# Kernel tuning notes

Hardware: AMD Instinct MI355X
Metric: run time of the kernel (lower is better)

The kernel has to match this reference:

```python
import jax, jax.numpy as jnp
import numpy as np

TOPK = 3
IOU_THRESHOLD = 0.5


def setup_inputs() -> dict:
    key = jax.random.key(0)
    k0, k1, k2, k3 = jax.random.split(key, 4)
    S, N, TGT_PER_VID = 256, 128, 4
    M = S * TGT_PER_VID          # 1024 target moments total
    P = N * N                    # 16384 valid proposals (mask2d all ones)
    start_offset = jax.random.normal(k0, (S, P), dtype=jnp.float32) * 0.1
    end_offset = jax.random.normal(k1, (S, P), dtype=jnp.float32) * 0.1
    # target moments: (start, end) in [0,1], start <= end
    tgt_moments = jnp.sort(jax.random.uniform(k2, (M, 2), dtype=jnp.float32), axis=1)
    num_targets = jnp.full((S,), TGT_PER_VID, dtype=jnp.int32)  # sums to M
    iou2ds = jax.random.uniform(k3, (M, N, N), dtype=jnp.float32)
    mask2d = jnp.ones((N, N), dtype=bool)
    return {
        "start_offset": start_offset,
        "end_offset": end_offset,
        "tgt_moments": tgt_moments,
        "num_targets": num_targets,
        "iou2ds": iou2ds,
        "mask2d": mask2d,
    }


def reference(start_offset, end_offset, tgt_moments, num_targets, iou2ds, mask2d):
    M, N, _ = iou2ds.shape
    S, P = start_offset.shape
    # map each of the M targets back to its source video (repeat_interleave)
    scatter_m2s = jnp.repeat(jnp.arange(S), num_targets, total_repeat_length=M)
    so = start_offset[scatter_m2s]  # [M, P]
    eo = end_offset[scatter_m2s]    # [M, P]
    # row-major nonzero positions of mask2d (== torch masked_select ordering)
    rows, cols = jnp.nonzero(mask2d, size=P)
    iou1ds = iou2ds[:, rows, cols]  # [M, P]
    # top-k scatter mask + IoU-threshold mask
    _, topk_idx = jax.lax.top_k(iou1ds, TOPK)  # [M, TOPK]
    target_mask = jnp.zeros((M, P), dtype=start_offset.dtype)
    target_mask = target_mask.at[jnp.arange(M)[:, None], topk_idx].set(1.0)
    target_mask = jnp.where(iou1ds > IOU_THRESHOLD, 1.0, target_mask)
    # scores2ds_to_moments: proposal (row, col) -> moment (row/N, (col+1)/N)
    starts = rows.astype(start_offset.dtype) / N                 # [P]
    ends = (cols.astype(start_offset.dtype) + 1.0) / N           # [P]
    start_offset_target = tgt_moments[:, 0:1] - starts[None, :]  # [M, P]
    end_offset_target = tgt_moments[:, 1:2] - ends[None, :]      # [M, P]
    loss = jnp.abs(so - start_offset_target) + jnp.abs(eo - end_offset_target)
    return (loss * target_mask).sum() / target_mask.sum()
```

## Files before the change

### kernel.cpp

```cpp
#include <hip/hip_runtime.h>
#include <math.h>

#define TOPK_N 3
#define IOU_THR 0.5f
#define NCNT 8
#define THREADS 512
#define NW (THREADS / 64)
#define SENT 0x7fffffff

__device__ __forceinline__ bool better(float va, int ia, float vb, int ib) {
    return (va > vb) || (va == vb && ia < ib);
}

__device__ __forceinline__ void merge3(float& a0, float& a1, float& a2,
                                       int& x0, int& x1, int& x2,
                                       float b0, float b1, float b2,
                                       int y0, int y1, int y2) {
    bool t0 = better(a0, x0, b0, y0);
    float ov0 = t0 ? a0 : b0;  int oi0 = t0 ? x0 : y0;
    float ahv = t0 ? a1 : a0;  int ahi = t0 ? x1 : x0;
    float a2v = t0 ? a2 : a1;  int a2i = t0 ? x2 : x1;
    float bhv = t0 ? b0 : b1;  int bhi = t0 ? y0 : y1;
    float b2v = t0 ? b1 : b2;  int b2i = t0 ? y1 : y2;
    bool t1 = better(ahv, ahi, bhv, bhi);
    float ov1 = t1 ? ahv : bhv; int oi1 = t1 ? ahi : bhi;
    float cav = t1 ? a2v : ahv; int cai = t1 ? a2i : ahi;
    float cbv = t1 ? bhv : b2v; int cbi = t1 ? bhi : b2i;
    bool t2 = better(cav, cai, cbv, cbi);
    a0 = ov0; a1 = ov1; a2 = t2 ? cav : cbv;
    x0 = oi0; x1 = oi1; x2 = t2 ? cai : cbi;
}

__global__ void prep_kernel(const int* __restrict__ num_targets,
                            const int* __restrict__ mask2d,
                            int* __restrict__ scatter,
                            int* __restrict__ counts,
                            int S, int M, int P) {
    const int bid = blockIdx.x;
    const int tid = threadIdx.x;

    if (bid < NCNT) {
        const int P4 = P >> 2;
        const int4* __restrict__ m4 = (const int4*)mask2d;
        int c = 0;
        for (int q = bid * 256 + tid; q < P4; q += NCNT * 256) {
            const int4 v = m4[q];
            c += (v.x != 0) + (v.y != 0) + (v.z != 0) + (v.w != 0);
        }
        if (bid == 0) {
            for (int j = (P4 << 2) + tid; j < P; j += 256)
                c += (mask2d[j] != 0);
        }
        __shared__ int red[256];
        red[tid] = c;
        __syncthreads();
        for (int st = 128; st > 0; st >>= 1) {
            if (tid < st) red[tid] += red[tid + st];
            __syncthreads();
        }
        if (tid == 0) counts[bid] = red[0];
    } else {
        __shared__ int cum[1025];
        __shared__ int scn[256];
        const int chunk = (S + 255) / 256;
        const int sbase = tid * chunk;
        int local[4];
        int csum = 0;
        for (int k = 0; k < chunk && k < 4; ++k) {
            int s = sbase + k;
            int v = (s < S) ? num_targets[s] : 0;
            csum += v;
            local[k] = csum;
        }
        scn[tid] = csum;
        __syncthreads();
        for (int d = 1; d < 256; d <<= 1) {
            int v = scn[tid];
            int add = (tid >= d) ? scn[tid - d] : 0;
            __syncthreads();
            scn[tid] = v + add;
            __syncthreads();
        }
        {
            int excl = scn[tid] - csum;
            for (int k = 0; k < chunk && k < 4; ++k) {
                int s = sbase + k;
                if (s < S) cum[s + 1] = excl + local[k];
            }
            if (tid == 0) cum[0] = 0;
        }
        __syncthreads();
        const int total = cum[S];
        for (int m = tid; m < M; m += 256) {
            int mm = m;
            if (mm >= total) mm = (total > 0) ? (total - 1) : 0;
            int lo = 0, hi = S - 1;
            while (lo < hi) {
                int mid = (lo + hi) >> 1;
                if (cum[mid + 1] <= mm) lo = mid + 1; else hi = mid;
            }
            scatter[m] = lo;
        }
    }
}

__global__ void build_kernel(const int* __restrict__ counts,
                             const int* __restrict__ mask2d,
                             int* __restrict__ rcidx,
                             float* __restrict__ starts,
                             float* __restrict__ ends,
                             int* __restrict__ flag,
                             int N, int P) {
    const int tid = threadIdx.x;
    __shared__ int scan[256];

    scan[tid] = (tid < NCNT) ? counts[tid] : 0;
    __syncthreads();
    for (int st = 128; st > 0; st >>= 1) {
        if (tid < st) scan[tid] += scan[tid + st];
        __syncthreads();
    }
    const int K_all = scan[0];
    const int f = (K_all == P && (P & 3) == 0 && (N & (N - 1)) == 0 && N >= 4) ? 1 : 0;
    if (tid == 0) flag[0] = f;
    if (f) return;
    __syncthreads();

    const int per = (P + 255) / 256;
    const int base = tid * per;
    int cnt = 0;
    for (int k = 0; k < per; ++k) {
        int j = base + k;
        if (j < P && mask2d[j] != 0) cnt++;
    }
    scan[tid] = cnt;
    __syncthreads();
    for (int d = 1; d < 256; d <<= 1) {
        int v = scan[tid];
        int add = (tid >= d) ? scan[tid - d] : 0;
        __syncthreads();
        scan[tid] = v + add;
        __syncthreads();
    }
    const int K = scan[255];
    int pos = scan[tid] - cnt;

    const float fN = (float)N;
    for (int k = 0; k < per; ++k) {
        int j = base + k;
        if (j < P && mask2d[j] != 0) {
            int r = j / N;
            int c = j - r * N;
            rcidx[pos]  = j;
            starts[pos] = (float)r / fN;
            ends[pos]   = (float)(c + 1) / fN;
            pos++;
        }
    }
    __syncthreads();
    for (int j = K + tid; j < P; j += 256) {
        rcidx[j]  = 0;
        starts[j] = 0.0f;
        ends[j]   = 1.0f / fN;
    }
}

__global__ __launch_bounds__(THREADS, 8)
void loss_kernel(const float* __restrict__ start_offset,
                 const float* __restrict__ end_offset,
                 const float* __restrict__ tgt_moments,
                 const int* __restrict__ scatter,
                 const float* __restrict__ iou2ds,
                 const int* __restrict__ rcidx,
                 const float* __restrict__ starts,
                 const float* __restrict__ ends,
                 double* __restrict__ psum,
                 int* __restrict__ pcnt,
                 const int* __restrict__ flag,
                 int P, int M, int N) {
    const int bid = blockIdx.x;
    const int m = ((M & 7) == 0) ? ((bid & 7) * (M >> 3) + (bid >> 3)) : bid;
    const int tid = threadIdx.x;
    const int s   = scatter[m];
    const int fp  = flag[0];

    const float* __restrict__ so_row  = start_offset + (size_t)s * P;
    const float* __restrict__ eo_row  = end_offset   + (size_t)s * P;
    const float* __restrict__ iou_row = iou2ds       + (size_t)m * P;
    const float tgt0 = tgt_moments[2 * m];
    const float tgt1 = tgt_moments[2 * m + 1];

    const int   lgN  = 31 - __clz(N);
    const float invN = 1.0f / (float)N;

    float lsum = 0.0f;
    int   lcnt = 0;

    float v0 = -INFINITY, v1 = -INFINITY, v2 = -INFINITY;
    int   i0 = SENT, i1 = SENT, i2 = SENT;

#define PROC(v, jj, so_, eo_, A_, B_)                                       \
    do {                                                                    \
        const bool b0 = (v) > v0;                                           \
        const bool b1 = (v) > v1;                                           \
        const bool b2 = (v) > v2;                                           \
        v2 = b1 ? v1 : (b2 ? (v) : v2);  i2 = b1 ? i1 : (b2 ? (jj) : i2);   \
        v1 = b0 ? v0 : (b1 ? (v) : v1);  i1 = b0 ? i0 : (b1 ? (jj) : i1);   \
        v0 = b0 ? (v) : v0;              i0 = b0 ? (jj) : i0;               \
        const bool sel = (v) > IOU_THR;                                     \
        const float l_ = fabsf((so_) - (A_)) + fabsf((eo_) - (B_));         \
        lsum += sel ? l_ : 0.0f;                                            \
        lcnt += sel ? 1 : 0;                                                \
    } while (0)

#define PROC4(vi, vs, ve, q)                                                \
    do {                                                                    \
        const int j_  = (q) << 2;                                           \
        const int r_  = j_ >> lgN;                                          \
        const int c_  = j_ & (N - 1);                                       \
        const float A_  = tgt0 - (float)r_ * invN;      \
        const float en0 = (float)(c_ + 1) * invN;     \
        PROC((vi).x, j_ + 0, (vs).x, (ve).x, A_, tgt1 - en0);               \
        PROC((vi).y, j_ + 1, (vs).y, (ve).y, A_, tgt1 - (en0 + invN));      \
        PROC((vi).z, j_ + 2, (vs).z, (ve).z, A_, tgt1 - (en0 + 2.0f*invN)); \
        PROC((vi).w, j_ + 3, (vs).w, (ve).w, A_, tgt1 - (en0 + 3.0f*invN)); \
    } while (0)

    if (fp && (P & (8 * THREADS - 1)) == 0) {
        const float4* __restrict__ iou4 = (const float4*)iou_row;
        const float4* __restrict__ so4  = (const float4*)so_row;
        const float4* __restrict__ eo4  = (const float4*)eo_row;
        const int ITERS = P >> (2 + 1 + 9);
        int qA = tid;
        for (int it = 0; it < ITERS; ++it) {
            const int qB = qA + THREADS;
            const float4 iA = iou4[qA]; const float4 iB = iou4[qB];
            const float4 sA = so4[qA];  const float4 sB = so4[qB];
            const float4 eA = eo4[qA];  const float4 eB = eo4[qB];
            PROC4(iA, sA, eA, qA);
            PROC4(iB, sB, eB, qB);
            qA += 2 * THREADS;
        }
    } else if (fp) {
        const float4* __restrict__ iou4 = (const float4*)iou_row;
        const float4* __restrict__ so4  = (const float4*)so_row;
        const float4* __restrict__ eo4  = (const float4*)eo_row;
        const int P4 = P >> 2;
        for (int q = tid; q < P4; q += THREADS) {
            const float4 vi = iou4[q];
            const float4 vs = so4[q];
            const float4 ve = eo4[q];
            PROC4(vi, vs, ve, q);
        }
    } else {
        for (int j = tid; j < P; j += THREADS) {
            const int   idx = rcidx[j];
            const float v   = iou_row[idx];
            const float A_  = tgt0 - starts[j];
            const float B_  = tgt1 - ends[j];
            PROC(v, j, so_row[j], eo_row[j], A_, B_);
        }
    }
#undef PROC4
#undef PROC

    for (int d = 1; d < 64; d <<= 1) {
        float bv0 = __shfl_xor(v0, d), bv1 = __shfl_xor(v1, d), bv2 = __shfl_xor(v2, d);
        int   by0 = __shfl_xor(i0, d), by1 = __shfl_xor(i1, d), by2 = __shfl_xor(i2, d);
        merge3(v0, v1, v2, i0, i1, i2, bv0, bv1, bv2, by0, by1, by2);
    }
    double dsum = (double)lsum;
    for (int d = 1; d < 64; d <<= 1) dsum += __shfl_xor(dsum, d);
    for (int d = 1; d < 64; d <<= 1) lcnt += __shfl_xor(lcnt, d);

    __shared__ float  wv[NW][3];
    __shared__ int    wi[NW][3];
    __shared__ double wsum[NW];
    __shared__ int    wcnt[NW];
    const int wid  = tid >> 6;
    const int lane = tid & 63;
    if (lane == 0) {
        wv[wid][0] = v0; wv[wid][1] = v1; wv[wid][2] = v2;
        wi[wid][0] = i0; wi[wid][1] = i1; wi[wid][2] = i2;
        wsum[wid] = dsum; wcnt[wid] = lcnt;
    }
    __syncthreads();

    if (tid == 0) {
        float a0 = wv[0][0], a1 = wv[0][1], a2 = wv[0][2];
        int   x0 = wi[0][0], x1 = wi[0][1], x2 = wi[0][2];
        double S = wsum[0];
        int    C = wcnt[0];
        for (int w = 1; w < NW; ++w) {
            merge3(a0, a1, a2, x0, x1, x2,
                   wv[w][0], wv[w][1], wv[w][2],
                   wi[w][0], wi[w][1], wi[w][2]);
            S += wsum[w];
            C += wcnt[w];
        }
#define ADDTOP(vk, jk)                                                      \
        do {                                                                \
            if ((jk) != SENT && !((vk) > IOU_THR)) {                        \
                float st_, en_;                                             \
                if (fp) {                                                   \
                    int r_ = (jk) >> lgN, c_ = (jk) & (N - 1);              \
                    st_ = (float)r_ * invN; en_ = (float)(c_ + 1) * invN;   \
                } else { st_ = starts[jk]; en_ = ends[jk]; }                \
                S += (double)(fabsf(so_row[jk] - (tgt0 - st_)) +            \
                              fabsf(eo_row[jk] - (tgt1 - en_)));            \
                C += 1;                                                     \
            }                                                               \
        } while (0)
        ADDTOP(a0, x0);
        ADDTOP(a1, x1);
        ADDTOP(a2, x2);
#undef ADDTOP
        psum[bid] = S;
        pcnt[bid] = C;
    }
}

__global__ void finalize_kernel(const double* __restrict__ psum,
                                const int* __restrict__ pcnt,
                                int M, float* __restrict__ out) {
    __shared__ double sd[256];
    __shared__ int    sc[256];
    const int tid = threadIdx.x;
    double a = 0.0;
    int    c = 0;
    for (int i = tid; i < M; i += 256) { a += psum[i]; c += pcnt[i]; }
    sd[tid] = a; sc[tid] = c;
    __syncthreads();
    for (int str = 128; str > 0; str >>= 1) {
        if (tid < str) { sd[tid] += sd[tid + str]; sc[tid] += sc[tid + str]; }
        __syncthreads();
    }
    if (tid == 0) out[0] = (float)(sd[0] / (double)sc[0]);
}

extern "C" void kernel_launch(void* const* d_in, const int* in_sizes, int n_in,
                              void* d_out, int out_size, void* d_ws, size_t ws_size,
                              hipStream_t stream) {
    const float* start_offset = (const float*)d_in[0];
    const float* end_offset   = (const float*)d_in[1];
    const float* tgt_moments  = (const float*)d_in[2];
    const int*   num_targets  = (const int*)d_in[3];
    const float* iou2ds       = (const float*)d_in[4];
    const int*   mask2d       = (const int*)d_in[5];

    const int S = in_sizes[3];
    const int M = in_sizes[2] / 2;
    const int P = in_sizes[0] / S;
    const int NN = in_sizes[5];
    int N = 1;
    while ((long long)N * N < (long long)NN) N++;

    char* ws = (char*)d_ws;
    size_t off = 0;
    int*    flag    = (int*)(ws + off);    off += 16;
    int*    counts  = (int*)(ws + off);    off += (NCNT * 4 + 15) & ~(size_t)15;
    int*    scatter = (int*)(ws + off);    off += ((size_t)M * 4 + 15) & ~(size_t)15;
    int*    rcidx   = (int*)(ws + off);    off += ((size_t)P * 4 + 15) & ~(size_t)15;
    float*  starts  = (float*)(ws + off);  off += ((size_t)P * 4 + 15) & ~(size_t)15;
    float*  ends    = (float*)(ws + off);  off += ((size_t)P * 4 + 15) & ~(size_t)15;
    double* psum    = (double*)(ws + off); off += ((size_t)M * 8 + 15) & ~(size_t)15;
    int*    pcnt    = (int*)(ws + off);    off += ((size_t)M * 4 + 15) & ~(size_t)15;

    prep_kernel<<<NCNT + 1, 256, 0, stream>>>(num_targets, mask2d, scatter, counts,
                                              S, M, P);
    build_kernel<<<1, 256, 0, stream>>>(counts, mask2d, rcidx, starts, ends, flag, N, P);
    loss_kernel<<<M, THREADS, 0, stream>>>(start_offset, end_offset, tgt_moments,
                                           scatter, iou2ds, rcidx, starts, ends,
                                           psum, pcnt, flag, P, M, N);
    finalize_kernel<<<1, 256, 0, stream>>>(psum, pcnt, M, (float*)d_out);
}
```

Baseline: 34.55 us.

## Double-buffer float4 loads in main loop, use med3 for top-3 insertion

```diff
diff --git a/kernel.cpp b/kernel.cpp
--- a/kernel.cpp
+++ b/kernel.cpp
@@ -165,7 +165,7 @@
     }
 }
 
-__global__ __launch_bounds__(THREADS, 8)
+__global__ __launch_bounds__(THREADS, 4)
 void loss_kernel(const float* __restrict__ start_offset,
                  const float* __restrict__ end_offset,
                  const float* __restrict__ tgt_moments,
@@ -204,9 +204,13 @@
         const bool b0 = (v) > v0;                                           \
         const bool b1 = (v) > v1;                                           \
         const bool b2 = (v) > v2;                                           \
-        v2 = b1 ? v1 : (b2 ? (v) : v2);  i2 = b1 ? i1 : (b2 ? (jj) : i2);   \
-        v1 = b0 ? v0 : (b1 ? (v) : v1);  i1 = b0 ? i0 : (b1 ? (jj) : i1);   \
-        v0 = b0 ? (v) : v0;              i0 = b0 ? (jj) : i0;               \
+        const float nv0 = fmaxf(v0, (v));                                   \
+        const float nv1 = __builtin_amdgcn_fmed3f((v), v0, v1);             \
+        const float nv2 = __builtin_amdgcn_fmed3f((v), v1, v2);             \
+        i2 = b1 ? i1 : (b2 ? (jj) : i2);                                    \
+        i1 = b0 ? i0 : (b1 ? (jj) : i1);                                    \
+        i0 = b0 ? (jj) : i0;                                                \
+        v0 = nv0; v1 = nv1; v2 = nv2;                                       \
         const bool sel = (v) > IOU_THR;                                     \
         const float l_ = fabsf((so_) - (A_)) + fabsf((eo_) - (B_));         \
         lsum += sel ? l_ : 0.0f;                                            \
@@ -226,21 +230,48 @@
         PROC((vi).w, j_ + 3, (vs).w, (ve).w, A_, tgt1 - (en0 + 3.0f*invN)); \
     } while (0)
 
-    if (fp && (P & (8 * THREADS - 1)) == 0) {
+    if (fp && (P % (16 * THREADS)) == 0) {
         const float4* __restrict__ iou4 = (const float4*)iou_row;
         const float4* __restrict__ so4  = (const float4*)so_row;
         const float4* __restrict__ eo4  = (const float4*)eo_row;
-        const int ITERS = P >> (2 + 1 + 9);
-        int qA = tid;
-        for (int it = 0; it < ITERS; ++it) {
-            const int qB = qA + THREADS;
-            const float4 iA = iou4[qA]; const float4 iB = iou4[qB];
-            const float4 sA = so4[qA];  const float4 sB = so4[qB];
-            const float4 eA = eo4[qA];  const float4 eB = eo4[qB];
-            PROC4(iA, sA, eA, qA);
-            PROC4(iB, sB, eB, qB);
-            qA += 2 * THREADS;
-        }
+        const int G = P / (16 * THREADS);
+        float4 iA0, iA1, iA2, iA3, sA0, sA1, sA2, sA3, eA0, eA1, eA2, eA3;
+        float4 iB0, iB1, iB2, iB3, sB0, sB1, sB2, sB3, eB0, eB1, eB2, eB3;
+
+#define LOADG(T, g)                                                         \
+    do {                                                                    \
+        const int qb_ = (g) * (4 * THREADS) + tid;                          \
+        i##T##0 = iou4[qb_];               i##T##1 = iou4[qb_ + THREADS];   \
+        i##T##2 = iou4[qb_ + 2*THREADS];   i##T##3 = iou4[qb_ + 3*THREADS]; \
+        s##T##0 = so4[qb_];                s##T##1 = so4[qb_ + THREADS];    \
+        s##T##2 = so4[qb_ + 2*THREADS];    s##T##3 = so4[qb_ + 3*THREADS];  \
+        e##T##0 = eo4[qb_];                e##T##1 = eo4[qb_ + THREADS];    \
+        e##T##2 = eo4[qb_ + 2*THREADS];    e##T##3 = eo4[qb_ + 3*THREADS];  \
+    } while (0)
+
+#define COMPG(T, g)                                                         \
+    do {                                                                    \
+        const int qb_ = (g) * (4 * THREADS) + tid;                          \
+        PROC4(i##T##0, s##T##0, e##T##0, qb_);                              \
+        PROC4(i##T##1, s##T##1, e##T##1, qb_ + THREADS);                    \
+        PROC4(i##T##2, s##T##2, e##T##2, qb_ + 2*THREADS);                  \
+        PROC4(i##T##3, s##T##3, e##T##3, qb_ + 3*THREADS);                  \
+    } while (0)
+
+        LOADG(A, 0);
+        int g = 0;
+        while (true) {
+            if (g + 1 < G) LOADG(B, g + 1);
+            COMPG(A, g);
+            ++g;
+            if (g >= G) break;
+            if (g + 1 < G) LOADG(A, g + 1);
+            COMPG(B, g);
+            ++g;
+            if (g >= G) break;
+        }
+#undef COMPG
+#undef LOADG
     } else if (fp) {
         const float4* __restrict__ iou4 = (const float4*)iou_row;
         const float4* __restrict__ so4  = (const float4*)so_row;
```

Measured after the change: 51.42 us. 1.49x slower.

## Stage loss-kernel loads through LDS with async double buffering per wave

Applied to the files above, without the earlier changes.

```diff
diff --git a/kernel.cpp b/kernel.cpp
--- a/kernel.cpp
+++ b/kernel.cpp
@@ -1,11 +1,8 @@
 #include <hip/hip_runtime.h>
 #include <math.h>
 
-#define TOPK_N 3
 #define IOU_THR 0.5f
 #define NCNT 8
-#define THREADS 512
-#define NW (THREADS / 64)
 #define SENT 0x7fffffff
 
 __device__ __forceinline__ bool better(float va, int ia, float vb, int ib) {
@@ -31,6 +28,13 @@
     x0 = oi0; x1 = oi1; x2 = t2 ? cai : cbi;
 }
 
+__device__ __forceinline__ void gload16(const void* g, void* l) {
+    __builtin_amdgcn_global_load_lds(
+        (const __attribute__((address_space(1))) unsigned int*)g,
+        (__attribute__((address_space(3))) unsigned int*)l,
+        16, 0, 0);
+}
+
 __global__ void prep_kernel(const int* __restrict__ num_targets,
                             const int* __restrict__ mask2d,
                             int* __restrict__ scatter,
@@ -165,7 +169,7 @@
     }
 }
 
-__global__ __launch_bounds__(THREADS, 8)
+__global__ __launch_bounds__(256)
 void loss_kernel(const float* __restrict__ start_offset,
                  const float* __restrict__ end_offset,
                  const float* __restrict__ tgt_moments,
@@ -181,8 +185,8 @@
     const int bid = blockIdx.x;
     const int m = ((M & 7) == 0) ? ((bid & 7) * (M >> 3) + (bid >> 3)) : bid;
     const int tid = threadIdx.x;
+    const int fp  = flag[0];
     const int s   = scatter[m];
-    const int fp  = flag[0];
 
     const float* __restrict__ so_row  = start_offset + (size_t)s * P;
     const float* __restrict__ eo_row  = end_offset   + (size_t)s * P;
@@ -193,67 +197,103 @@
     const int   lgN  = 31 - __clz(N);
     const float invN = 1.0f / (float)N;
 
+    float v0 = -INFINITY, v1 = -INFINITY, v2 = -INFINITY;
+    int   i0 = SENT, i1 = SENT, i2 = SENT;
     float lsum = 0.0f;
     int   lcnt = 0;
-
-    float v0 = -INFINITY, v1 = -INFINITY, v2 = -INFINITY;
-    int   i0 = SENT, i1 = SENT, i2 = SENT;
 
 #define PROC(v, jj, so_, eo_, A_, B_)                                       \
     do {                                                                    \
         const bool b0 = (v) > v0;                                           \
         const bool b1 = (v) > v1;                                           \
         const bool b2 = (v) > v2;                                           \
-        v2 = b1 ? v1 : (b2 ? (v) : v2);  i2 = b1 ? i1 : (b2 ? (jj) : i2);   \
-        v1 = b0 ? v0 : (b1 ? (v) : v1);  i1 = b0 ? i0 : (b1 ? (jj) : i1);   \
-        v0 = b0 ? (v) : v0;              i0 = b0 ? (jj) : i0;               \
+        const float nv0 = fmaxf(v0, (v));                                   \
+        const float nv1 = __builtin_amdgcn_fmed3f((v), v0, v1);             \
+        const float nv2 = __builtin_amdgcn_fmed3f((v), v1, v2);             \
+        i2 = b1 ? i1 : (b2 ? (jj) : i2);                                    \
+        i1 = b0 ? i0 : (b1 ? (jj) : i1);                                    \
+        i0 = b0 ? (jj) : i0;                                                \
+        v0 = nv0; v1 = nv1; v2 = nv2;                                       \
         const bool sel = (v) > IOU_THR;                                     \
         const float l_ = fabsf((so_) - (A_)) + fabsf((eo_) - (B_));         \
         lsum += sel ? l_ : 0.0f;                                            \
         lcnt += sel ? 1 : 0;                                                \
     } while (0)
 
-#define PROC4(vi, vs, ve, q)                                                \
+#define PROC4(vi, vs, ve, qf4)                                              \
     do {                                                                    \
-        const int j_  = (q) << 2;                                           \
-        const int r_  = j_ >> lgN;                                          \
-        const int c_  = j_ & (N - 1);                                       \
-        const float A_  = tgt0 - (float)r_ * invN;      \
-        const float en0 = (float)(c_ + 1) * invN;     \
+        const int j_ = (qf4) << 2;                                          \
+        const int r_ = j_ >> lgN;                                           \
+        const int c_ = j_ & (N - 1);                                        \
+        const float A_  = tgt0 - (float)r_ * invN;                          \
+        const float en0 = (float)(c_ + 1) * invN;                           \
         PROC((vi).x, j_ + 0, (vs).x, (ve).x, A_, tgt1 - en0);               \
         PROC((vi).y, j_ + 1, (vs).y, (ve).y, A_, tgt1 - (en0 + invN));      \
         PROC((vi).z, j_ + 2, (vs).z, (ve).z, A_, tgt1 - (en0 + 2.0f*invN)); \
         PROC((vi).w, j_ + 3, (vs).w, (ve).w, A_, tgt1 - (en0 + 3.0f*invN)); \
     } while (0)
 
-    if (fp && (P & (8 * THREADS - 1)) == 0) {
-        const float4* __restrict__ iou4 = (const float4*)iou_row;
-        const float4* __restrict__ so4  = (const float4*)so_row;
-        const float4* __restrict__ eo4  = (const float4*)eo_row;
-        const int ITERS = P >> (2 + 1 + 9);
-        int qA = tid;
-        for (int it = 0; it < ITERS; ++it) {
-            const int qB = qA + THREADS;
-            const float4 iA = iou4[qA]; const float4 iB = iou4[qB];
-            const float4 sA = so4[qA];  const float4 sB = so4[qB];
-            const float4 eA = eo4[qA];  const float4 eB = eo4[qB];
-            PROC4(iA, sA, eA, qA);
-            PROC4(iB, sB, eB, qB);
-            qA += 2 * THREADS;
-        }
+    __shared__ float4 stg[4][2][3][128];
+
+    const bool deep = fp && ((P & 2047) == 0);
+
+    if (deep) {
+        const int wid  = tid >> 6;
+        const int lane = tid & 63;
+        const float4* __restrict__ io4 = (const float4*)iou_row;
+        const float4* __restrict__ so4 = (const float4*)so_row;
+        const float4* __restrict__ eo4 = (const float4*)eo_row;
+        const int wq0   = wid * (P >> 4);
+        const int iters = (P >> 4) >> 7;
+
+#define STAGE(B, T)                                                         \
+    do {                                                                    \
+        const int qb = wq0 + (T) * 128;                                     \
+        gload16(io4 + qb + lane,      &stg[wid][B][0][0]);                  \
+        gload16(io4 + qb + 64 + lane, &stg[wid][B][0][64]);                 \
+        gload16(so4 + qb + lane,      &stg[wid][B][1][0]);                  \
+        gload16(so4 + qb + 64 + lane, &stg[wid][B][1][64]);                 \
+        gload16(eo4 + qb + lane,      &stg[wid][B][2][0]);                  \
+        gload16(eo4 + qb + 64 + lane, &stg[wid][B][2][64]);                 \
+    } while (0)
+
+        STAGE(0, 0);
+        for (int t = 0; t < iters; ++t) {
+            const int b = t & 1;
+            if (t + 1 < iters) {
+                asm volatile("s_waitcnt lgkmcnt(0)" ::: "memory");
+                __builtin_amdgcn_sched_barrier(0);
+                STAGE(b ^ 1, t + 1);
+                asm volatile("s_waitcnt vmcnt(6)" ::: "memory");
+            } else {
+                asm volatile("s_waitcnt vmcnt(0)" ::: "memory");
+            }
+            __builtin_amdgcn_sched_barrier(0);
+
+            const int q  = wq0 + t * 128 + lane;
+            const float4 vi0 = stg[wid][b][0][lane];
+            const float4 vi1 = stg[wid][b][0][64 + lane];
+            const float4 vs0 = stg[wid][b][1][lane];
+            const float4 vs1 = stg[wid][b][1][64 + lane];
+            const float4 ve0 = stg[wid][b][2][lane];
+            const float4 ve1 = stg[wid][b][2][64 + lane];
+            PROC4(vi0, vs0, ve0, q);
+            PROC4(vi1, vs1, ve1, q + 64);
+        }
+#undef STAGE
     } else if (fp) {
-        const float4* __restrict__ iou4 = (const float4*)iou_row;
-        const float4* __restrict__ so4  = (const float4*)so_row;
-        const float4* __restrict__ eo4  = (const float4*)eo_row;
+        const float4* __restrict__ io4 = (const float4*)iou_row;
+        const float4* __restrict__ so4 = (const float4*)so_row;
+        const float4* __restrict__ eo4 = (const float4*)eo_row;
         const int P4 = P >> 2;
-        for (int q = tid; q < P4; q += THREADS) {
-            const float4 vi = iou4[q];
+        for (int q = tid; q < P4; q += 256) {
+            const float4 vi = io4[q];
             const float4 vs = so4[q];
             const float4 ve = eo4[q];
             PROC4(vi, vs, ve, q);
         }
     } else {
-        for (int j = tid; j < P; j += THREADS) {
+        for (int j = tid; j < P; j += 256) {
             const int   idx = rcidx[j];
             const float v   = iou_row[idx];
             const float A_  = tgt0 - starts[j];
@@ -265,18 +305,18 @@
 #undef PROC
 
     for (int d = 1; d < 64; d <<= 1) {
-        float bv0 = __shfl_xor(v0, d), bv1 = __shfl_xor(v1, d), bv2 = __shfl_xor(v2, d);
-        int   by0 = __shfl_xor(i0, d), by1 = __shfl_xor(i1, d), by2 = __shfl_xor(i2, d);
-        merge3(v0, v1, v2, i0, i1, i2, bv0, bv1, bv2, by0, by1, by2);
+        float b0v = __shfl_xor(v0, d), b1v = __shfl_xor(v1, d), b2v = __shfl_xor(v2, d);
+        int   y0 = __shfl_xor(i0, d), y1 = __shfl_xor(i1, d), y2 = __shfl_xor(i2, d);
+        merge3(v0, v1, v2, i0, i1, i2, b0v, b1v, b2v, y0, y1, y2);
     }
     double dsum = (double)lsum;
     for (int d = 1; d < 64; d <<= 1) dsum += __shfl_xor(dsum, d);
     for (int d = 1; d < 64; d <<= 1) lcnt += __shfl_xor(lcnt, d);
 
-    __shared__ float  wv[NW][3];
-    __shared__ int    wi[NW][3];
-    __shared__ double wsum[NW];
-    __shared__ int    wcnt[NW];
+    __shared__ float  wv[4][3];
+    __shared__ int    wi[4][3];
+    __shared__ double wsum[4];
+    __shared__ int    wcnt[4];
     const int wid  = tid >> 6;
     const int lane = tid & 63;
     if (lane == 0) {
@@ -289,14 +329,14 @@
     if (tid == 0) {
         float a0 = wv[0][0], a1 = wv[0][1], a2 = wv[0][2];
         int   x0 = wi[0][0], x1 = wi[0][1], x2 = wi[0][2];
-        double S = wsum[0];
-        int    C = wcnt[0];
-        for (int w = 1; w < NW; ++w) {
+        double Sm = wsum[0];
+        int    Cm = wcnt[0];
+        for (int w = 1; w < 4; ++w) {
             merge3(a0, a1, a2, x0, x1, x2,
                    wv[w][0], wv[w][1], wv[w][2],
                    wi[w][0], wi[w][1], wi[w][2]);
-            S += wsum[w];
-            C += wcnt[w];
+            Sm += wsum[w];
+            Cm += wcnt[w];
         }
 #define ADDTOP(vk, jk)                                                      \
         do {                                                                \
@@ -306,17 +346,17 @@
                     int r_ = (jk) >> lgN, c_ = (jk) & (N - 1);              \
                     st_ = (float)r_ * invN; en_ = (float)(c_ + 1) * invN;   \
                 } else { st_ = starts[jk]; en_ = ends[jk]; }                \
-                S += (double)(fabsf(so_row[jk] - (tgt0 - st_)) +            \
-                              fabsf(eo_row[jk] - (tgt1 - en_)));            \
-                C += 1;                                                     \
+                Sm += (double)(fabsf(so_row[jk] - (tgt0 - st_)) +           \
+                               fabsf(eo_row[jk] - (tgt1 - en_)));           \
+                Cm += 1;                                                    \
             }                                                               \
         } while (0)
         ADDTOP(a0, x0);
         ADDTOP(a1, x1);
         ADDTOP(a2, x2);
 #undef ADDTOP
-        psum[bid] = S;
-        pcnt[bid] = C;
+        psum[m] = Sm;
+        pcnt[m] = Cm;
     }
 }
 
@@ -369,8 +409,8 @@
     prep_kernel<<<NCNT + 1, 256, 0, stream>>>(num_targets, mask2d, scatter, counts,
                                               S, M, P);
     build_kernel<<<1, 256, 0, stream>>>(counts, mask2d, rcidx, starts, ends, flag, N, P);
-    loss_kernel<<<M, THREADS, 0, stream>>>(start_offset, end_offset, tgt_moments,
-                                           scatter, iou2ds, rcidx, starts, ends,
-                                           psum, pcnt, flag, P, M, N);
+    loss_kernel<<<M, 256, 0, stream>>>(start_offset, end_offset, tgt_moments,
+                                       scatter, iou2ds, rcidx, starts, ends,
+                                       psum, pcnt, flag, P, M, N);
     finalize_kernel<<<1, 256, 0, stream>>>(psum, pcnt, M, (float*)d_out);
 }
```

New measurement: 41.90 us. 1.21x slower.
